# Performance work log

Hardware: AMD Instinct MI355X
Metric: run time of the kernel (lower is better)

Reference implementation:

```python
import math
import jax, jax.numpy as jnp
import numpy as np

DMODEL = 1024
NUM_HEADS = 16
HEAD_DIM = DMODEL // NUM_HEADS
MAX_LEN = 1024


def setup_inputs() -> dict:
    key = jax.random.key(0)
    ks = jax.random.split(key, 10)
    bs, S = 4, 1024
    s = 0.02
    return {
        "query": jax.random.normal(ks[0], (bs, S, DMODEL), jnp.float32),
        "key": jax.random.normal(ks[1], (bs, S, DMODEL), jnp.float32),
        "value": jax.random.normal(ks[2], (bs, S, DMODEL), jnp.float32),
        "Wq": jax.random.normal(ks[3], (DMODEL, DMODEL), jnp.float32) * s,
        "bq": jnp.zeros((DMODEL,), jnp.float32),
        "Wk": jax.random.normal(ks[4], (DMODEL, DMODEL), jnp.float32) * s,
        "bk": jnp.zeros((DMODEL,), jnp.float32),
        "Wv": jax.random.normal(ks[5], (DMODEL, DMODEL), jnp.float32) * s,
        "bv": jnp.zeros((DMODEL,), jnp.float32),
        # relative embedding table: (H, 2*max_len-1+2, head_dim)
        "Er": jax.random.normal(ks[6], (NUM_HEADS, 2 * MAX_LEN + 1, HEAD_DIM), jnp.float32),
    }


def _skew(QEr):
    # Music-Transformer skew trick. QEr: (bs, H, S, L) with L = 2S-1.
    bs, H, S, L = QEr.shape
    x = jnp.pad(QEr, ((0, 0), (0, 0), (0, 0), (0, 1)))          # (bs,H,S,L+1)
    x = x.reshape(bs, H, S * (L + 1))
    x = jnp.pad(x, ((0, 0), (0, 0), (0, L - S)))
    x = x.reshape(bs, H, S + 1, L)
    return x[:, :, :S, -S:]                                      # (bs,H,S,S)


def reference(query, key, value, Wq, bq, Wk, bk, Wv, bv, Er):
    bs, S, D = query.shape
    H, hd = NUM_HEADS, HEAD_DIM
    # torch nn.Linear: x @ W.T + b
    q = (query @ Wq.T + bq).reshape(bs, S, H, hd).transpose(0, 2, 1, 3)  # (bs,H,S,hd)
    k = (key @ Wk.T + bk).reshape(bs, S, H, hd).transpose(0, 2, 1, 3)    # (bs,H,S,hd)
    v = (value @ Wv.T + bv).reshape(bs, S, H, hd).transpose(0, 2, 1, 3)  # (bs,H,S,hd)
    # slice Er for src_len <= max_len: rows [max_len-S, max_len+S-1) -> (H, 2S-1, hd)
    Er_t = Er[:, max(0, MAX_LEN - S):min(2 * MAX_LEN - 1, MAX_LEN + S - 1), :]
    QEr = jnp.einsum('bhsd,hld->bhsl', q, Er_t)                  # (bs,H,S,2S-1)
    Srel = _skew(QEr)                                            # (bs,H,S,S)
    attn = (jnp.einsum('bhsd,bhtd->bhst', q, k) + Srel) / math.sqrt(hd)
    attn = jax.nn.softmax(attn, axis=-1)
    out = jnp.einsum('bhst,bhtd->bhsd', attn, v)                 # (bs,H,S,hd)
    out = out.transpose(0, 2, 1, 3).reshape(bs, S, D)
    return out, attn
```

## Files before the change

### kernel.cpp

```cpp
#include <hip/hip_runtime.h>
#include <hip/hip_fp16.h>

#define SQ   1024
#define DM   1024
#define NH   16
#define HD   64
#define BSZ  4

typedef _Float16 f16;
typedef f16  f16x8 __attribute__((ext_vector_type(8)));
typedef f16  f16x4 __attribute__((ext_vector_type(4)));
typedef float f32x4 __attribute__((ext_vector_type(4)));

#define MFMA16(a,b,c) __builtin_amdgcn_mfma_f32_16x16x32_f16(a,b,c,0,0,0)

#define GLOAD_LDS(g, l) __builtin_amdgcn_global_load_lds( \
    (const __attribute__((address_space(1))) void*)(g), \
    (__attribute__((address_space(3))) void*)(l), 16, 0, 0)

#define XIN16OFF  0
#define W16OFF    12582912
#define ER16OFF   15728640
#define QKV16OFF  17826816
#define VTOFF     30409728

__global__ __launch_bounds__(256) void cvt_all(
    const float* __restrict__ q, const float* __restrict__ k, const float* __restrict__ v,
    const float* __restrict__ wq, const float* __restrict__ wk, const float* __restrict__ wv,
    const float* __restrict__ er, f16* __restrict__ ws)
{
    int z = blockIdx.z;
    const float* src; f16* dst; int n;
    if (z < 3)      { src = (z==0)?q:((z==1)?k:v);    dst = ws + (size_t)z*4194304;              n = 4194304; }
    else if (z < 6) { src = (z==3)?wq:((z==4)?wk:wv); dst = ws + W16OFF + (size_t)(z-3)*1048576; n = 1048576; }
    else            { src = er;                        dst = ws + ER16OFF;                        n = 2098176; }
    int idx = (blockIdx.x*256 + threadIdx.x) * 8;
    if (idx >= n) return;
    float4 a = *(const float4*)&src[idx];
    float4 b = *(const float4*)&src[idx+4];
    f16x8 o;
    o[0]=(f16)a.x; o[1]=(f16)a.y; o[2]=(f16)a.z; o[3]=(f16)a.w;
    o[4]=(f16)b.x; o[5]=(f16)b.y; o[6]=(f16)b.z; o[7]=(f16)b.w;
    *(f16x8*)&dst[idx] = o;
}

__global__ __launch_bounds__(256) void proj_gemm(
    f16* __restrict__ ws, const float* __restrict__ bq,
    const float* __restrict__ bk, const float* __restrict__ bv)
{
    int z = blockIdx.z;
    const f16* X = ws + XIN16OFF + (size_t)z*4194304;
    const f16* W = ws + W16OFF   + (size_t)z*1048576;
    const float* bias = (z==0)?bq:((z==1)?bk:bv);
    f16* dst = ws + QKV16OFF + (size_t)z*4194304;

    int n0 = blockIdx.x * 128, m0 = blockIdx.y * 128;
    int tid = threadIdx.x, lane = tid & 63, w = tid >> 6;
    int wm = (w >> 1) * 64, wn = (w & 1) * 64;

    __shared__ f16 As[128*32];
    __shared__ f16 Bs[128*32];

    f32x4 acc[4][4];
    #pragma unroll
    for (int a=0;a<4;++a)
        #pragma unroll
        for (int b=0;b<4;++b) { acc[a][b][0]=0.f;acc[a][b][1]=0.f;acc[a][b][2]=0.f;acc[a][b][3]=0.f; }

    int srow0 = tid >> 2, srow1 = srow0 + 64, skc = (tid & 3) * 8;
    int fr = lane & 15, fk = (lane >> 4) << 3;

    for (int k0 = 0; k0 < 1024; k0 += 32) {
        __syncthreads();
        GLOAD_LDS(&X[(size_t)(m0+srow0)*1024 + k0 + skc], &As[srow0*32 + skc]);
        GLOAD_LDS(&X[(size_t)(m0+srow1)*1024 + k0 + skc], &As[srow1*32 + skc]);
        GLOAD_LDS(&W[(size_t)(n0+srow0)*1024 + k0 + skc], &Bs[srow0*32 + skc]);
        GLOAD_LDS(&W[(size_t)(n0+srow1)*1024 + k0 + skc], &Bs[srow1*32 + skc]);
        __syncthreads();
        f16x8 af[4], bf[4];
        #pragma unroll
        for (int a=0;a<4;++a) af[a] = *(const f16x8*)&As[(wm + a*16 + fr)*32 + fk];
        #pragma unroll
        for (int b=0;b<4;++b) bf[b] = *(const f16x8*)&Bs[(wn + b*16 + fr)*32 + fk];
        #pragma unroll
        for (int a=0;a<4;++a)
            #pragma unroll
            for (int b=0;b<4;++b)
                acc[a][b] = MFMA16(af[a], bf[b], acc[a][b]);
    }

    int coln = lane & 15, rq = (lane >> 4) << 2;
    #pragma unroll
    for (int tb = 0; tb < 4; ++tb) {
        int j = n0 + wn + tb*16 + coln;
        int hh = j >> 6, dd = j & 63;
        float bsv = bias[j];
        #pragma unroll
        for (int ta = 0; ta < 4; ++ta) {
            #pragma unroll
            for (int r = 0; r < 4; ++r) {
                int m = m0 + wm + ta*16 + rq + r;
                int bidx = m >> 10, s = m & 1023;
                dst[((size_t)(bidx*16 + hh)*1024 + s)*64 + dd] = (f16)(acc[ta][tb][r] + bsv);
            }
        }
    }
}

__global__ __launch_bounds__(256) void transpose_v(f16* __restrict__ ws)
{
    const f16* v = ws + QKV16OFF + 2*4194304 + (size_t)blockIdx.y*65536;
    f16* o       = ws + VTOFF               + (size_t)blockIdx.y*65536;
    int s0 = blockIdx.x << 6;
    __shared__ f16 t[64][72];
    int tid = threadIdx.x;
    int r = tid >> 2, c = (tid & 3) << 4;
    f16x8 a = *(const f16x8*)&v[(size_t)(s0+r)*64 + c];
    f16x8 b = *(const f16x8*)&v[(size_t)(s0+r)*64 + c + 8];
    #pragma unroll
    for (int j = 0; j < 8; ++j) { t[r][c+j] = a[j]; t[r][c+8+j] = b[j]; }
    __syncthreads();
    int dr = tid >> 2, sc0 = (tid & 3) << 4;
    f16x8 o1, o2;
    #pragma unroll
    for (int j = 0; j < 8; ++j) { o1[j] = t[sc0+j][dr]; o2[j] = t[sc0+8+j][dr]; }
    *(f16x8*)&o[(size_t)dr*1024 + s0 + sc0]     = o1;
    *(f16x8*)&o[(size_t)dr*1024 + s0 + sc0 + 8] = o2;
}

__global__ __launch_bounds__(256, 4) void attn_pv(
    const f16* __restrict__ ws, float* __restrict__ attn, float* __restrict__ out)
{
    const f16* qkv = ws + QKV16OFF;
    const f16* er  = ws + ER16OFF;
    int bh = blockIdx.y, h = bh & 15, b = bh >> 4;
    int s0 = blockIdx.x << 4;
    int tid = threadIdx.x, lane = tid & 63, w = tid >> 6;

    const f16* qb  = qkv + (size_t)bh * 65536;
    const f16* kb  = qkv + 4194304 + (size_t)bh * 65536;
    const f16* vtb = ws + VTOFF + (size_t)bh * 65536;
    const f16* E   = er + (size_t)h * 2049 * 64;

    __shared__ __align__(16) f16 lds_pool[4*16*264];
    __shared__ float red[16][4];
    f16* P16 = lds_pool + w * (16*264);

    int fr = lane & 15, fk = (lane >> 4) << 3;
    f16x8 qf0 = *(const f16x8*)&qb[(s0+fr)*64 + fk];
    f16x8 qf1 = *(const f16x8*)&qb[(s0+fr)*64 + fk + 32];

    int tbase = w << 8;
    int l0 = 1008 + tbase - s0;

    f16x8 kf0 = *(const f16x8*)&kb[(tbase+fr)*64 + fk];
    f16x8 kf1 = *(const f16x8*)&kb[(tbase+fr)*64 + fk + 32];
    f16x8 e0a = *(const f16x8*)&E[(size_t)(l0+fr)*64 + fk];
    f16x8 e0b = *(const f16x8*)&E[(size_t)(l0+fr)*64 + fk + 32];
    f16x8 e1a = *(const f16x8*)&E[(size_t)(l0+16+fr)*64 + fk];
    f16x8 e1b = *(const f16x8*)&E[(size_t)(l0+16+fr)*64 + fk + 32];

    float rs[4];
    rs[0]=0.f; rs[1]=0.f; rs[2]=0.f; rs[3]=0.f;

    #pragma unroll
    for (int i = 0; i < 16; ++i) {
        f16x8 nk0, nk1, nea, neb;
        if (i < 15) {
            int t0n = tbase + ((i+1) << 4);
            nk0 = *(const f16x8*)&kb[(t0n+fr)*64 + fk];
            nk1 = *(const f16x8*)&kb[(t0n+fr)*64 + fk + 32];
            int ln = l0 + ((i+2) << 4);
            nea = *(const f16x8*)&E[(size_t)(ln+fr)*64 + fk];
            neb = *(const f16x8*)&E[(size_t)(ln+fr)*64 + fk + 32];
        }

        f32x4 c; c[0]=0.f;c[1]=0.f;c[2]=0.f;c[3]=0.f;
        c = MFMA16(qf0, kf0, c);
        c = MFMA16(qf1, kf1, c);

        f32x4 r0; r0[0]=0.f;r0[1]=0.f;r0[2]=0.f;r0[3]=0.f;
        f32x4 r1; r1[0]=0.f;r1[1]=0.f;r1[2]=0.f;r1[3]=0.f;
        r0 = MFMA16(qf0, e0a, r0); r0 = MFMA16(qf1, e0b, r0);
        r1 = MFMA16(qf0, e1a, r1); r1 = MFMA16(qf1, e1b, r1);

        #pragma unroll
        for (int r = 0; r < 4; ++r) {
            int shat = ((lane >> 4) << 2) + r;
            int jj = (lane & 15) - shat + 15;
            int addr = ((lane & 48) | (jj & 15)) << 2;
            float m = ((lane & 15) >= 15 - shat) ? r0[r] : r1[r];
            float g = __int_as_float(__builtin_amdgcn_ds_bpermute(addr, __float_as_int(m)));
            float sv = (c[r] + g) * 0.125f;
            float e  = __expf(sv);
            rs[r] += e;
            P16[shat*264 + (i<<4) + (lane & 15)] = (f16)e;
        }

        if (i < 15) {
            kf0 = nk0; kf1 = nk1;
            e0a = e1a; e0b = e1b; e1a = nea; e1b = neb;
        }
    }

    #pragma unroll
    for (int r = 0; r < 4; ++r) {
        float s = rs[r];
        s += __shfl_xor(s, 1); s += __shfl_xor(s, 2);
        s += __shfl_xor(s, 4); s += __shfl_xor(s, 8);
        rs[r] = s;
    }
    if ((lane & 15) == 0) {
        #pragma unroll
        for (int r = 0; r < 4; ++r) red[((lane>>4)<<2)+r][w] = rs[r];
    }
    __syncthreads();

    {
        float* outb = attn + ((size_t)bh * 1024 + s0) * 1024;
        int arow = tid >> 4;
        int ac0  = (tid & 15) << 2;
        float iv = 1.f / (red[arow][0] + red[arow][1] + red[arow][2] + red[arow][3]);
        #pragma unroll
        for (int it = 0; it < 16; ++it) {
            int col = ac0 + it*64;
            const f16* p = &lds_pool[(col >> 8)*(16*264) + arow*264 + (col & 255)];
            f16x4 p4 = *(const f16x4*)p;
            float4 o4;
            o4.x = (float)p4[0] * iv; o4.y = (float)p4[1] * iv;
            o4.z = (float)p4[2] * iv; o4.w = (float)p4[3] * iv;
            *(float4*)&outb[(size_t)arow*1024 + col] = o4;
        }
    }

    f32x4 oacc[4];
    #pragma unroll
    for (int nb=0;nb<4;++nb) { oacc[nb][0]=0.f;oacc[nb][1]=0.f;oacc[nb][2]=0.f;oacc[nb][3]=0.f; }
    f16x8 bcur[4], bnxt[4];
    #pragma unroll
    for (int nb = 0; nb < 4; ++nb)
        bcur[nb] = *(const f16x8*)&vtb[(size_t)((nb<<4)+fr)*1024 + tbase + fk];
    #pragma unroll
    for (int kc = 0; kc < 8; ++kc) {
        if (kc < 7) {
            #pragma unroll
            for (int nb = 0; nb < 4; ++nb)
                bnxt[nb] = *(const f16x8*)&vtb[(size_t)((nb<<4)+fr)*1024 + tbase + ((kc+1)<<5) + fk];
        }
        f16x8 af = *(const f16x8*)&P16[fr*264 + (kc<<5) + fk];
        #pragma unroll
        for (int nb = 0; nb < 4; ++nb)
            oacc[nb] = MFMA16(af, bcur[nb], oacc[nb]);
        if (kc < 7) {
            #pragma unroll
            for (int nb = 0; nb < 4; ++nb) bcur[nb] = bnxt[nb];
        }
    }

    __syncthreads();
    float* Ored = (float*)lds_pool;
    {
        float iv2[4];
        #pragma unroll
        for (int r = 0; r < 4; ++r) {
            int rw = ((lane>>4)<<2)+r;
            iv2[r] = 1.f / (red[rw][0] + red[rw][1] + red[rw][2] + red[rw][3]);
        }
        #pragma unroll
        for (int nb = 0; nb < 4; ++nb)
            #pragma unroll
            for (int r = 0; r < 4; ++r) {
                int rw = ((lane>>4)<<2)+r;
                Ored[w*1024 + rw*64 + (nb<<4) + (lane & 15)] = oacc[nb][r] * iv2[r];
            }
    }
    __syncthreads();
    {
        int frow = tid >> 4, fc = (tid & 15) << 2;
        float4 s4;
        s4.x = Ored[frow*64+fc+0] + Ored[1024+frow*64+fc+0] + Ored[2048+frow*64+fc+0] + Ored[3072+frow*64+fc+0];
        s4.y = Ored[frow*64+fc+1] + Ored[1024+frow*64+fc+1] + Ored[2048+frow*64+fc+1] + Ored[3072+frow*64+fc+1];
        s4.z = Ored[frow*64+fc+2] + Ored[1024+frow*64+fc+2] + Ored[2048+frow*64+fc+2] + Ored[3072+frow*64+fc+2];
        s4.w = Ored[frow*64+fc+3] + Ored[1024+frow*64+fc+3] + Ored[2048+frow*64+fc+3] + Ored[3072+frow*64+fc+3];
        *(float4*)&out[((size_t)b*1024 + s0 + frow)*1024 + h*64 + fc] = s4;
    }
}

extern "C" void kernel_launch(void* const* d_in, const int* in_sizes, int n_in,
                              void* d_out, int out_size, void* d_ws, size_t ws_size,
                              hipStream_t stream) {
    const float* query = (const float*)d_in[0];
    const float* key   = (const float*)d_in[1];
    const float* value = (const float*)d_in[2];
    const float* Wq    = (const float*)d_in[3];
    const float* bq    = (const float*)d_in[4];
    const float* Wk    = (const float*)d_in[5];
    const float* bk    = (const float*)d_in[6];
    const float* Wv    = (const float*)d_in[7];
    const float* bv    = (const float*)d_in[8];

    f16*   ws   = (f16*)d_ws;
    float* out  = (float*)d_out;
    float* attn = out + 4194304;

    cvt_all    <<<dim3(2048, 1, 7), 256, 0, stream>>>(query, key, value, Wq, Wk, Wv,
                                                      (const float*)d_in[9], ws);
    proj_gemm  <<<dim3(8, 32, 3),   256, 0, stream>>>(ws, bq, bk, bv);
    transpose_v<<<dim3(16, 64),     256, 0, stream>>>(ws);
    attn_pv    <<<dim3(64, 64),     256, 0, stream>>>(ws, attn, out);
}
```

Baseline: 553.4 us.

## Recompute scores in second pass, swizzle projection LDS tiles, remap GEMM block order

The attention kernel no longer holds a full 16x1024 fp16 probability tile in LDS. It runs a first pass that only gathers row sums, then recomputes QK^T and the relative-position scores in a second pass. That pass writes the normalized probabilities straight to global memory and feeds a small double-slot LDS stage into the PV MFMAs. The aim is lower LDS use so occupancy can rise (launch bounds raised to 5), at the cost of doubling the score MFMAs and the K/Er loads. The projection GEMM moves to a K-tile of 64 with an XOR-swizzled LDS layout to avoid bank conflicts, plus a remapped block order for better L2 locality.

```diff
diff --git a/kernel.cpp b/kernel.cpp
--- a/kernel.cpp
+++ b/kernel.cpp
@@ -54,12 +54,15 @@
     const float* bias = (z==0)?bq:((z==1)?bk:bv);
     f16* dst = ws + QKV16OFF + (size_t)z*4194304;
 
-    int n0 = blockIdx.x * 128, m0 = blockIdx.y * 128;
+    int flat = blockIdx.y * 8 + blockIdx.x;
+    int f = ((flat & 7) << 5) + (flat >> 3);
+    int n0 = (f & 7) * 128, m0 = (f >> 3) * 128;
+
     int tid = threadIdx.x, lane = tid & 63, w = tid >> 6;
     int wm = (w >> 1) * 64, wn = (w & 1) * 64;
 
-    __shared__ f16 As[128*32];
-    __shared__ f16 Bs[128*32];
+    __shared__ f16 As[128*64];
+    __shared__ f16 Bs[128*64];
 
     f32x4 acc[4][4];
     #pragma unroll
@@ -67,26 +70,40 @@
         #pragma unroll
         for (int b=0;b<4;++b) { acc[a][b][0]=0.f;acc[a][b][1]=0.f;acc[a][b][2]=0.f;acc[a][b][3]=0.f; }
 
-    int srow0 = tid >> 2, srow1 = srow0 + 64, skc = (tid & 3) * 8;
-    int fr = lane & 15, fk = (lane >> 4) << 3;
-
-    for (int k0 = 0; k0 < 1024; k0 += 32) {
+    int srow = tid >> 3;
+    int sdst = (tid & 7) << 3;
+    int ssrc = (((tid & 7) ^ ((tid >> 3) & 7)) << 3);
+
+    int fr = lane & 15, fkh = (lane >> 4) << 3;
+    int ra0 = (fkh)      ^ ((fr & 7) << 3);
+    int ra1 = (fkh + 32) ^ ((fr & 7) << 3);
+
+    for (int k0 = 0; k0 < 1024; k0 += 64) {
         __syncthreads();
-        GLOAD_LDS(&X[(size_t)(m0+srow0)*1024 + k0 + skc], &As[srow0*32 + skc]);
-        GLOAD_LDS(&X[(size_t)(m0+srow1)*1024 + k0 + skc], &As[srow1*32 + skc]);
-        GLOAD_LDS(&W[(size_t)(n0+srow0)*1024 + k0 + skc], &Bs[srow0*32 + skc]);
-        GLOAD_LDS(&W[(size_t)(n0+srow1)*1024 + k0 + skc], &Bs[srow1*32 + skc]);
+        #pragma unroll
+        for (int u = 0; u < 4; ++u) {
+            GLOAD_LDS(&X[(size_t)(m0+srow+32*u)*1024 + k0 + ssrc], &As[(srow+32*u)*64 + sdst]);
+            GLOAD_LDS(&W[(size_t)(n0+srow+32*u)*1024 + k0 + ssrc], &Bs[(srow+32*u)*64 + sdst]);
+        }
         __syncthreads();
-        f16x8 af[4], bf[4];
-        #pragma unroll
-        for (int a=0;a<4;++a) af[a] = *(const f16x8*)&As[(wm + a*16 + fr)*32 + fk];
-        #pragma unroll
-        for (int b=0;b<4;++b) bf[b] = *(const f16x8*)&Bs[(wn + b*16 + fr)*32 + fk];
+        f16x8 a0[4], a1[4], b0[4], b1[4];
+        #pragma unroll
+        for (int a=0;a<4;++a) {
+            a0[a] = *(const f16x8*)&As[(wm + a*16 + fr)*64 + ra0];
+            a1[a] = *(const f16x8*)&As[(wm + a*16 + fr)*64 + ra1];
+        }
+        #pragma unroll
+        for (int bb=0;bb<4;++bb) {
+            b0[bb] = *(const f16x8*)&Bs[(wn + bb*16 + fr)*64 + ra0];
+            b1[bb] = *(const f16x8*)&Bs[(wn + bb*16 + fr)*64 + ra1];
+        }
         #pragma unroll
         for (int a=0;a<4;++a)
             #pragma unroll
-            for (int b=0;b<4;++b)
-                acc[a][b] = MFMA16(af[a], bf[b], acc[a][b]);
+            for (int bb=0;bb<4;++bb) {
+                acc[a][bb] = MFMA16(a0[a], b0[bb], acc[a][bb]);
+                acc[a][bb] = MFMA16(a1[a], b1[bb], acc[a][bb]);
+            }
     }
 
     int coln = lane & 15, rq = (lane >> 4) << 2;
@@ -128,7 +145,7 @@
     *(f16x8*)&o[(size_t)dr*1024 + s0 + sc0 + 8] = o2;
 }
 
-__global__ __launch_bounds__(256, 4) void attn_pv(
+__global__ __launch_bounds__(256, 5) void attn_pv(
     const f16* __restrict__ ws, float* __restrict__ attn, float* __restrict__ out)
 {
     const f16* qkv = ws + QKV16OFF;
@@ -142,11 +159,12 @@
     const f16* vtb = ws + VTOFF + (size_t)bh * 65536;
     const f16* E   = er + (size_t)h * 2049 * 64;
 
-    __shared__ __align__(16) f16 lds_pool[4*16*264];
+    __shared__ __align__(16) float lds_pool[4096];
     __shared__ float red[16][4];
-    f16* P16 = lds_pool + w * (16*264);
+    f16* pstage = (f16*)lds_pool + w * 640;
 
     int fr = lane & 15, fk = (lane >> 4) << 3;
+    int hi = lane >> 4;
     f16x8 qf0 = *(const f16x8*)&qb[(s0+fr)*64 + fk];
     f16x8 qf1 = *(const f16x8*)&qb[(s0+fr)*64 + fk + 32];
 
@@ -160,8 +178,7 @@
     f16x8 e1a = *(const f16x8*)&E[(size_t)(l0+16+fr)*64 + fk];
     f16x8 e1b = *(const f16x8*)&E[(size_t)(l0+16+fr)*64 + fk + 32];
 
-    float rs[4];
-    rs[0]=0.f; rs[1]=0.f; rs[2]=0.f; rs[3]=0.f;
+    float rs[4] = {0.f, 0.f, 0.f, 0.f};
 
     #pragma unroll
     for (int i = 0; i < 16; ++i) {
@@ -175,32 +192,25 @@
             neb = *(const f16x8*)&E[(size_t)(ln+fr)*64 + fk + 32];
         }
 
-        f32x4 c; c[0]=0.f;c[1]=0.f;c[2]=0.f;c[3]=0.f;
+        f32x4 c = {0.f,0.f,0.f,0.f};
         c = MFMA16(qf0, kf0, c);
         c = MFMA16(qf1, kf1, c);
-
-        f32x4 r0; r0[0]=0.f;r0[1]=0.f;r0[2]=0.f;r0[3]=0.f;
-        f32x4 r1; r1[0]=0.f;r1[1]=0.f;r1[2]=0.f;r1[3]=0.f;
+        f32x4 r0 = {0.f,0.f,0.f,0.f};
+        f32x4 r1 = {0.f,0.f,0.f,0.f};
         r0 = MFMA16(qf0, e0a, r0); r0 = MFMA16(qf1, e0b, r0);
         r1 = MFMA16(qf0, e1a, r1); r1 = MFMA16(qf1, e1b, r1);
 
         #pragma unroll
         for (int r = 0; r < 4; ++r) {
-            int shat = ((lane >> 4) << 2) + r;
-            int jj = (lane & 15) - shat + 15;
+            int shat = (hi << 2) + r;
+            int jj = fr - shat + 15;
             int addr = ((lane & 48) | (jj & 15)) << 2;
-            float m = ((lane & 15) >= 15 - shat) ? r0[r] : r1[r];
+            float m = (fr >= 15 - shat) ? r0[r] : r1[r];
             float g = __int_as_float(__builtin_amdgcn_ds_bpermute(addr, __float_as_int(m)));
-            float sv = (c[r] + g) * 0.125f;
-            float e  = __expf(sv);
-            rs[r] += e;
-            P16[shat*264 + (i<<4) + (lane & 15)] = (f16)e;
-        }
-
-        if (i < 15) {
-            kf0 = nk0; kf1 = nk1;
-            e0a = e1a; e0b = e1b; e1a = nea; e1b = neb;
-        }
+            rs[r] += __expf((c[r] + g) * 0.125f);
+        }
+
+        if (i < 15) { kf0 = nk0; kf1 = nk1; e0a = e1a; e0b = e1b; e1a = nea; e1b = neb; }
     }
 
     #pragma unroll
@@ -210,28 +220,20 @@
         s += __shfl_xor(s, 4); s += __shfl_xor(s, 8);
         rs[r] = s;
     }
-    if ((lane & 15) == 0) {
-        #pragma unroll
-        for (int r = 0; r < 4; ++r) red[((lane>>4)<<2)+r][w] = rs[r];
+    if (fr == 0) {
+        #pragma unroll
+        for (int r = 0; r < 4; ++r) red[(hi<<2)+r][w] = rs[r];
     }
     __syncthreads();
 
-    {
-        float* outb = attn + ((size_t)bh * 1024 + s0) * 1024;
-        int arow = tid >> 4;
-        int ac0  = (tid & 15) << 2;
-        float iv = 1.f / (red[arow][0] + red[arow][1] + red[arow][2] + red[arow][3]);
-        #pragma unroll
-        for (int it = 0; it < 16; ++it) {
-            int col = ac0 + it*64;
-            const f16* p = &lds_pool[(col >> 8)*(16*264) + arow*264 + (col & 255)];
-            f16x4 p4 = *(const f16x4*)p;
-            float4 o4;
-            o4.x = (float)p4[0] * iv; o4.y = (float)p4[1] * iv;
-            o4.z = (float)p4[2] * iv; o4.w = (float)p4[3] * iv;
-            *(float4*)&outb[(size_t)arow*1024 + col] = o4;
-        }
-    }
+    float inv4[4];
+    #pragma unroll
+    for (int r = 0; r < 4; ++r) {
+        int rw = (hi<<2)+r;
+        inv4[r] = 1.f / (red[rw][0] + red[rw][1] + red[rw][2] + red[rw][3]);
+    }
+
+    float* arow0 = attn + ((size_t)bh*1024 + s0 + (hi<<2))*1024 + tbase + fr;
 
     f32x4 oacc[4];
     #pragma unroll
@@ -240,40 +242,63 @@
     #pragma unroll
     for (int nb = 0; nb < 4; ++nb)
         bcur[nb] = *(const f16x8*)&vtb[(size_t)((nb<<4)+fr)*1024 + tbase + fk];
-    #pragma unroll
-    for (int kc = 0; kc < 8; ++kc) {
-        if (kc < 7) {
+
+    #pragma unroll
+    for (int i = 0; i < 16; ++i) {
+        int t0 = tbase + (i << 4);
+        f16x8 pk0 = *(const f16x8*)&kb[(t0+fr)*64 + fk];
+        f16x8 pk1 = *(const f16x8*)&kb[(t0+fr)*64 + fk + 32];
+        int la = l0 + (i << 4);
+        f16x8 pea = *(const f16x8*)&E[(size_t)(la+fr)*64 + fk];
+        f16x8 peb = *(const f16x8*)&E[(size_t)(la+fr)*64 + fk + 32];
+        f16x8 pfa = *(const f16x8*)&E[(size_t)(la+16+fr)*64 + fk];
+        f16x8 pfb = *(const f16x8*)&E[(size_t)(la+16+fr)*64 + fk + 32];
+
+        f32x4 c = {0.f,0.f,0.f,0.f};
+        c = MFMA16(qf0, pk0, c);
+        c = MFMA16(qf1, pk1, c);
+        f32x4 r0 = {0.f,0.f,0.f,0.f};
+        f32x4 r1 = {0.f,0.f,0.f,0.f};
+        r0 = MFMA16(qf0, pea, r0); r0 = MFMA16(qf1, peb, r0);
+        r1 = MFMA16(qf0, pfa, r1); r1 = MFMA16(qf1, pfb, r1);
+
+        #pragma unroll
+        for (int r = 0; r < 4; ++r) {
+            int shat = (hi << 2) + r;
+            int jj = fr - shat + 15;
+            int addr = ((lane & 48) | (jj & 15)) << 2;
+            float m = (fr >= 15 - shat) ? r0[r] : r1[r];
+            float g = __int_as_float(__builtin_amdgcn_ds_bpermute(addr, __float_as_int(m)));
+            float en = __expf((c[r] + g) * 0.125f) * inv4[r];
+            arow0[(size_t)r*1024 + (i<<4)] = en;
+            pstage[shat*40 + ((i&1)<<4) + fr] = (f16)en;
+        }
+
+        if (i & 1) {
+            const int kc = i >> 1;
+            if (kc < 7) {
+                #pragma unroll
+                for (int nb = 0; nb < 4; ++nb)
+                    bnxt[nb] = *(const f16x8*)&vtb[(size_t)((nb<<4)+fr)*1024 + tbase + ((kc+1)<<5) + fk];
+            }
+            f16x8 af = *(const f16x8*)&pstage[fr*40 + fk];
             #pragma unroll
             for (int nb = 0; nb < 4; ++nb)
-                bnxt[nb] = *(const f16x8*)&vtb[(size_t)((nb<<4)+fr)*1024 + tbase + ((kc+1)<<5) + fk];
-        }
-        f16x8 af = *(const f16x8*)&P16[fr*264 + (kc<<5) + fk];
-        #pragma unroll
-        for (int nb = 0; nb < 4; ++nb)
-            oacc[nb] = MFMA16(af, bcur[nb], oacc[nb]);
-        if (kc < 7) {
-            #pragma unroll
-            for (int nb = 0; nb < 4; ++nb) bcur[nb] = bnxt[nb];
+                oacc[nb] = MFMA16(af, bcur[nb], oacc[nb]);
+            if (kc < 7) {
+                #pragma unroll
+                for (int nb = 0; nb < 4; ++nb) bcur[nb] = bnxt[nb];
+            }
         }
     }
 
     __syncthreads();
-    float* Ored = (float*)lds_pool;
-    {
-        float iv2[4];
-        #pragma unroll
-        for (int r = 0; r < 4; ++r) {
-            int rw = ((lane>>4)<<2)+r;
-            iv2[r] = 1.f / (red[rw][0] + red[rw][1] + red[rw][2] + red[rw][3]);
-        }
-        #pragma unroll
-        for (int nb = 0; nb < 4; ++nb)
-            #pragma unroll
-            for (int r = 0; r < 4; ++r) {
-                int rw = ((lane>>4)<<2)+r;
-                Ored[w*1024 + rw*64 + (nb<<4) + (lane & 15)] = oacc[nb][r] * iv2[r];
-            }
-    }
+    float* Ored = lds_pool;
+    #pragma unroll
+    for (int nb = 0; nb < 4; ++nb)
+        #pragma unroll
+        for (int r = 0; r < 4; ++r)
+            Ored[w*1024 + ((hi<<2)+r)*64 + (nb<<4) + fr] = oacc[nb][r];
     __syncthreads();
     {
         int frow = tid >> 4, fc = (tid & 15) << 2;
```

Measured after the change: 812.6 us. 46.8% more time.
